# Performance work log

Hardware: AMD Instinct MI355X
Metric: run time of the kernel (lower is better)

The kernel has to match this reference:

```python
import jax, jax.numpy as jnp
import numpy as np

D_MODEL = 2048
NUM_HEADS = 16
D_H = D_MODEL // NUM_HEADS
D_LATENT = 512
B, S = 2, 2048


def setup_inputs() -> dict:
    key = jax.random.key(0)
    ks = jax.random.split(key, 10)
    sd = lambda fan_in: 1.0 / np.sqrt(fan_in)
    x = jax.random.normal(ks[0], (B, S, D_MODEL), dtype=jnp.float32)
    # weights stored as [in, out] so y = x @ W + b (same math as nn.Linear)
    w_latent = jax.random.uniform(ks[1], (D_MODEL, D_LATENT), jnp.float32, -sd(D_MODEL), sd(D_MODEL))
    b_latent = jax.random.uniform(ks[2], (D_LATENT,), jnp.float32, -sd(D_MODEL), sd(D_MODEL))
    w_q = jax.random.uniform(ks[3], (D_MODEL, D_MODEL), jnp.float32, -sd(D_MODEL), sd(D_MODEL))
    b_q = jax.random.uniform(ks[4], (D_MODEL,), jnp.float32, -sd(D_MODEL), sd(D_MODEL))
    # per-head K/V projections batched into [H, d_latent, d_h]
    w_k = jax.random.uniform(ks[5], (NUM_HEADS, D_LATENT, D_H), jnp.float32, -sd(D_LATENT), sd(D_LATENT))
    b_k = jax.random.uniform(ks[6], (NUM_HEADS, D_H), jnp.float32, -sd(D_LATENT), sd(D_LATENT))
    w_v = jax.random.uniform(ks[7], (NUM_HEADS, D_LATENT, D_H), jnp.float32, -sd(D_LATENT), sd(D_LATENT))
    b_v = jax.random.uniform(ks[8], (NUM_HEADS, D_H), jnp.float32, -sd(D_LATENT), sd(D_LATENT))
    w_o = jax.random.uniform(ks[9], (D_MODEL, D_MODEL), jnp.float32, -sd(D_MODEL), sd(D_MODEL))
    b_o = jnp.zeros((D_MODEL,), jnp.float32)
    return {"x": x, "w_latent": w_latent, "b_latent": b_latent, "w_q": w_q, "b_q": b_q,
            "w_k": w_k, "b_k": b_k, "w_v": w_v, "b_v": b_v, "w_o": w_o, "b_o": b_o}


def reference(x, w_latent, b_latent, w_q, b_q, w_k, b_k, w_v, b_v, w_o, b_o):
    batch, seq, d = x.shape
    # latent KV compression: [B,S,d_latent]
    z = x @ w_latent + b_latent
    # queries: [B,H,S,d_h]
    q = (x @ w_q + b_q).reshape(batch, seq, NUM_HEADS, D_H).transpose(0, 2, 1, 3)
    # per-head K/V projections fused into one batched GEMM: [B,H,S,d_h]
    k = jnp.einsum('bsl,hld->bhsd', z, w_k) + b_k[None, :, None, :]
    v = jnp.einsum('bsl,hld->bhsd', z, w_v) + b_v[None, :, None, :]
    attn = jnp.einsum('bhqd,bhkd->bhqk', q, k) / np.sqrt(D_H).astype(np.float32)
    attn = jax.nn.softmax(attn, axis=-1)
    out = jnp.einsum('bhqk,bhkd->bhqd', attn, v)          # [B,H,S,d_h]
    out = out.transpose(0, 2, 1, 3).reshape(batch, seq, d)  # [B,S,D]
    return out @ w_o + b_o
```

## Files before the change

### kernel.cpp

```cpp
#include <hip/hip_runtime.h>
#include <hip/hip_bf16.h>

#define H_ATT   16
#define DH      128
#define DMODEL  2048
#define DLAT    512
#define NB      2
#define SEQ     2048
#define MROWS   (NB * SEQ)
#define NQZ     (DMODEL + DLAT)

#define SCL2 0.12751744f

typedef __bf16          bf16x8_t __attribute__((ext_vector_type(8)));
typedef float           f32x4_t  __attribute__((ext_vector_type(4)));
typedef unsigned short  u16x4_t  __attribute__((ext_vector_type(4)));

#if __has_builtin(__builtin_amdgcn_exp2f)
#define EXP2F(x) __builtin_amdgcn_exp2f(x)
#else
#define EXP2F(x) exp2f(x)
#endif

__device__ __forceinline__ unsigned short f2bf_u16(float f) {
  union { __bf16 b; unsigned short u; } cv; cv.b = (__bf16)f; return cv.u;
}

__device__ __forceinline__ void async_copy16(const __bf16* g, __bf16* l) {
  __builtin_amdgcn_global_load_lds(
      (const __attribute__((address_space(1))) unsigned int*)g,
      (__attribute__((address_space(3))) unsigned int*)l, 16, 0, 0);
}

__global__ void cast_f32_to_bf16(const float* __restrict__ in, __bf16* __restrict__ out, int n4) {
  int i = blockIdx.x * 256 + threadIdx.x;
  if (i >= n4) return;
  float4 v = ((const float4*)in)[i];
  ushort4 o;
  o.x = f2bf_u16(v.x); o.y = f2bf_u16(v.y); o.z = f2bf_u16(v.z); o.w = f2bf_u16(v.w);
  *((ushort4*)out + i) = o;
}

__global__ void transpose_cast(const float* __restrict__ in, __bf16* __restrict__ out,
                               int R, int C, float scale) {
  __shared__ float tile[32][33];
  in  += (size_t)blockIdx.z * R * C;
  out += (size_t)blockIdx.z * R * C;
  int c0 = blockIdx.x * 32, r0 = blockIdx.y * 32;
  int tx = threadIdx.x, ty = threadIdx.y;
  #pragma unroll
  for (int i = 0; i < 32; i += 8)
    tile[ty + i][tx] = in[(size_t)(r0 + ty + i) * C + (c0 + tx)];
  __syncthreads();
  #pragma unroll
  for (int i = 0; i < 32; i += 8)
    out[(size_t)(c0 + ty + i) * R + (r0 + tx)] = (__bf16)(tile[tx][ty + i] * scale);
}

__global__ void build_bqz(const float* __restrict__ b_q, const float* __restrict__ b_lat,
                          float* __restrict__ bqz) {
  int t = blockIdx.x * 256 + threadIdx.x;
  if (t < DMODEL)   bqz[t] = b_q[t] * SCL2;
  else if (t < NQZ) bqz[t] = b_lat[t - DMODEL];
}

#define BM 128
#define BN 128
#define BK 32

__device__ __forceinline__ void storec(float*  p, float v) { *p = v; }
__device__ __forceinline__ void storec(__bf16* p, float v) { *p = (__bf16)v; }

template <typename OutT, bool TRANSPV>
__global__ __launch_bounds__(256, 2)
void gemm_bt(const __bf16* __restrict__ A, const __bf16* __restrict__ Bt,
             const float* __restrict__ bias, OutT* __restrict__ C,
             int M, int N, int K, int lda, int ldc) {
  __shared__ __align__(16) __bf16 As[BM * BK];
  __shared__ __align__(16) __bf16 Bs[BN * BK];
  const int t    = threadIdx.x;
  const int wave = t >> 6, lane = t & 63;
  const int quad = lane >> 4, l16 = lane & 15;
  const int wm = (wave >> 1) * 64, wn = (wave & 1) * 64;
  const int row0 = blockIdx.y * BM, col0 = blockIdx.x * BN;
  const int srow = t >> 2, skc = t & 3;

  const __bf16* Ag  = A  + (size_t)(row0 + srow)      * lda + skc * 8;
  const __bf16* Ag2 = A  + (size_t)(row0 + srow + 64) * lda + skc * 8;
  const __bf16* Bg  = Bt + (size_t)(col0 + srow)      * K   + skc * 8;
  const __bf16* Bg2 = Bt + (size_t)(col0 + srow + 64) * K   + skc * 8;
  __bf16* Al  = As + t * 8;
  __bf16* Al2 = As + 2048 + t * 8;
  __bf16* Bl  = Bs + t * 8;
  __bf16* Bl2 = Bs + 2048 + t * 8;

  f32x4_t acc[4][4] = {};

  for (int k0 = 0; k0 < K; k0 += BK) {
    async_copy16(Ag  + k0, Al);
    async_copy16(Ag2 + k0, Al2);
    async_copy16(Bg  + k0, Bl);
    async_copy16(Bg2 + k0, Bl2);
    __syncthreads();
    bf16x8_t af[4], bfr[4];
    #pragma unroll
    for (int i = 0; i < 4; ++i)
      af[i] = *(const bf16x8_t*)(As + (wm + i * 16 + l16) * BK + quad * 8);
    #pragma unroll
    for (int j = 0; j < 4; ++j)
      bfr[j] = *(const bf16x8_t*)(Bs + (wn + j * 16 + l16) * BK + quad * 8);
    #pragma unroll
    for (int i = 0; i < 4; ++i)
      #pragma unroll
      for (int j = 0; j < 4; ++j)
        acc[i][j] = __builtin_amdgcn_mfma_f32_16x16x32_bf16(af[i], bfr[j], acc[i][j], 0, 0, 0);
    __syncthreads();
  }

  #pragma unroll
  for (int j = 0; j < 4; ++j) {
    int col = col0 + wn + j * 16 + l16;
    float bj = bias[col];
    #pragma unroll
    for (int i = 0; i < 4; ++i) {
      int row = row0 + wm + i * 16 + quad * 4;
      if (TRANSPV) {
        u16x4_t pw;
        #pragma unroll
        for (int r = 0; r < 4; ++r) pw[r] = f2bf_u16(acc[i][j][r] + bj);
        size_t bb = (size_t)(row >> 11);
        int s = row & (SEQ - 1);
        *(u16x4_t*)((__bf16*)C + bb * ((size_t)DMODEL * SEQ) + (size_t)col * SEQ + s) = pw;
      } else {
        #pragma unroll
        for (int r = 0; r < 4; ++r)
          storec(&C[(size_t)(row + r) * ldc + col], acc[i][j][r] + bj);
      }
    }
  }
}

#define TQ 128
#define TK 64

__global__ __launch_bounds__(256, 2)
void mla_attn(const __bf16* __restrict__ Qm, const __bf16* __restrict__ Km,
              const __bf16* __restrict__ Vtg, __bf16* __restrict__ Om) {
  __shared__ __align__(16) __bf16 Kls[16 * 512];
  __shared__ __align__(16) __bf16 Vls[2][16 * 512];
  __shared__ __align__(16) __bf16 Ps [16 * 512];
  __shared__ float Lbuf[2][TQ];

  const int t    = threadIdx.x;
  const int wave = t >> 6, lane = t & 63;
  const int quad = lane >> 4, l16 = lane & 15;
  const int wq = wave >> 1, wk = wave & 1, wd = wave & 1;
  const int h = blockIdx.y, b = blockIdx.z;
  const int q0 = blockIdx.x * TQ;
  const size_t kbase  = (size_t)b * SEQ * DMODEL + (size_t)h * DH;
  const size_t vtbase = ((size_t)b * DMODEL + (size_t)h * DH) * SEQ;
  const size_t obase  = (size_t)b * SEQ * DMODEL + (size_t)h * DH;

  bf16x8_t qf[4][4];
  #pragma unroll
  for (int nt = 0; nt < 4; ++nt) {
    const __bf16* qp = Qm + ((size_t)b * SEQ + q0 + wq * 64 + nt * 16 + l16) * NQZ
                       + (size_t)h * DH + quad * 8;
    #pragma unroll
    for (int kc = 0; kc < 4; ++kc)
      qf[nt][kc] = *(const bf16x8_t*)(qp + kc * 32);
  }

  auto stage = [&](int kt0, int vbuf) {
    #pragma unroll
    for (int i2 = 0; i2 < 4; ++i2) {
      int bidx = wave * 4 + i2;
      int mt = bidx >> 2, kc = bidx & 3;
      async_copy16(Km + kbase + (size_t)(kt0 + mt * 16 + l16) * DMODEL + kc * 32 + quad * 8,
                   Kls + bidx * 512 + lane * 8);
      int dt = bidx >> 1, ks = bidx & 1;
      async_copy16(Vtg + vtbase + (size_t)(dt * 16 + l16) * SEQ + kt0 + ks * 32 + quad * 8,
                   Vls[vbuf] + bidx * 512 + lane * 8);
    }
  };

  f32x4_t acc_o[4][4] = {};
  float l_part[4] = {0.f, 0.f, 0.f, 0.f};

  stage(0, 0);

  f32x4_t acc_s[2][4];
  for (int it = 0; it < SEQ / TK; ++it) {
    __syncthreads();

    if (it > 0) {
      const __bf16* Vb = Vls[(it - 1) & 1];
      #pragma unroll
      for (int ks = 0; ks < 2; ++ks) {
        bf16x8_t pf[4];
        #pragma unroll
        for (int mq = 0; mq < 4; ++mq)
          pf[mq] = *(const bf16x8_t*)(Ps + ((wq * 4 + mq) * 2 + ks) * 512 + lane * 8);
        #pragma unroll
        for (int nd = 0; nd < 4; ++nd) {
          bf16x8_t vf = *(const bf16x8_t*)(Vb + ((wd * 4 + nd) * 2 + ks) * 512 + lane * 8);
          #pragma unroll
          for (int mq = 0; mq < 4; ++mq)
            acc_o[mq][nd] = __builtin_amdgcn_mfma_f32_16x16x32_bf16(pf[mq], vf, acc_o[mq][nd], 0, 0, 0);
        }
      }
    }

    #pragma unroll
    for (int mtl = 0; mtl < 2; ++mtl)
      #pragma unroll
      for (int nt = 0; nt < 4; ++nt)
        acc_s[mtl][nt] = f32x4_t{0.f, 0.f, 0.f, 0.f};
    #pragma unroll
    for (int kc = 0; kc < 4; ++kc)
      #pragma unroll
      for (int mtl = 0; mtl < 2; ++mtl) {
        bf16x8_t kf = *(const bf16x8_t*)(Kls + ((wk * 2 + mtl) * 4 + kc) * 512 + lane * 8);
        #pragma unroll
        for (int nt = 0; nt < 4; ++nt)
          acc_s[mtl][nt] = __builtin_amdgcn_mfma_f32_16x16x32_bf16(kf, qf[nt][kc], acc_s[mtl][nt], 0, 0, 0);
      }

    __syncthreads();

    if (it + 1 < SEQ / TK) stage((it + 1) * TK, (it + 1) & 1);

    #pragma unroll
    for (int nt = 0; nt < 4; ++nt) {
      #pragma unroll
      for (int mtl = 0; mtl < 2; ++mtl) {
        u16x4_t pw;
        float s = 0.f;
        #pragma unroll
        for (int r = 0; r < 4; ++r) {
          float p = EXP2F(fminf(acc_s[mtl][nt][r], 80.f));
          s += p;
          pw[r] = f2bf_u16(p);
        }
        l_part[nt] += s;
        *(u16x4_t*)(Ps + ((wq * 4 + nt) * 2 + wk) * 512
                    + ((mtl * 2 + (quad >> 1)) * 16 + l16) * 8 + (quad & 1) * 4) = pw;
      }
    }
  }

  __syncthreads();
  {
    const __bf16* Vb = Vls[(SEQ / TK - 1) & 1];
    #pragma unroll
    for (int ks = 0; ks < 2; ++ks) {
      bf16x8_t pf[4];
      #pragma unroll
      for (int mq = 0; mq < 4; ++mq)
        pf[mq] = *(const bf16x8_t*)(Ps + ((wq * 4 + mq) * 2 + ks) * 512 + lane * 8);
      #pragma unroll
      for (int nd = 0; nd < 4; ++nd) {
        bf16x8_t vf = *(const bf16x8_t*)(Vb + ((wd * 4 + nd) * 2 + ks) * 512 + lane * 8);
        #pragma unroll
        for (int mq = 0; mq < 4; ++mq)
          acc_o[mq][nd] = __builtin_amdgcn_mfma_f32_16x16x32_bf16(pf[mq], vf, acc_o[mq][nd], 0, 0, 0);
      }
    }
  }

  #pragma unroll
  for (int nt = 0; nt < 4; ++nt) {
    float lp = l_part[nt];
    lp += __shfl_xor(lp, 16);
    lp += __shfl_xor(lp, 32);
    Lbuf[wk][wq * 64 + nt * 16 + l16] = lp;
  }
  __syncthreads();
  #pragma unroll
  for (int mq = 0; mq < 4; ++mq) {
    float li[4];
    #pragma unroll
    for (int r = 0; r < 4; ++r) {
      int qq = wq * 64 + mq * 16 + quad * 4 + r;
      li[r] = 1.f / (Lbuf[0][qq] + Lbuf[1][qq]);
    }
    #pragma unroll
    for (int nd = 0; nd < 4; ++nd) {
      int col = wd * 64 + nd * 16 + l16;
      #pragma unroll
      for (int r = 0; r < 4; ++r) {
        int row = q0 + wq * 64 + mq * 16 + quad * 4 + r;
        Om[obase + (size_t)row * DMODEL + col] = (__bf16)(acc_o[mq][nd][r] * li[r]);
      }
    }
  }
}

extern "C" void kernel_launch(void* const* d_in, const int* in_sizes, int n_in,
                              void* d_out, int out_size, void* d_ws, size_t ws_size,
                              hipStream_t stream) {
  (void)in_sizes; (void)n_in; (void)out_size; (void)ws_size;
  const float* x        = (const float*)d_in[0];
  const float* w_latent = (const float*)d_in[1];
  const float* b_latent = (const float*)d_in[2];
  const float* w_q      = (const float*)d_in[3];
  const float* b_q      = (const float*)d_in[4];
  const float* w_k      = (const float*)d_in[5];
  const float* b_k      = (const float*)d_in[6];
  const float* w_v      = (const float*)d_in[7];
  const float* b_v      = (const float*)d_in[8];
  const float* w_o      = (const float*)d_in[9];
  const float* b_o      = (const float*)d_in[10];
  float* out = (float*)d_out;

  __bf16* ws = (__bf16*)d_ws;
  __bf16* xb   = ws; ws += (size_t)MROWS * DMODEL;
  __bf16* wqzt = ws; ws += (size_t)NQZ * DMODEL;
  __bf16* wkt  = ws; ws += (size_t)DMODEL * DLAT;
  __bf16* wvt  = ws; ws += (size_t)DMODEL * DLAT;
  __bf16* wot  = ws; ws += (size_t)DMODEL * DMODEL;
  __bf16* qzb  = ws; ws += (size_t)MROWS * NQZ;
  __bf16* kb   = ws; ws += (size_t)MROWS * DMODEL;
  __bf16* vt   = ws; ws += (size_t)MROWS * DMODEL;
  __bf16* ao   = ws; ws += (size_t)MROWS * DMODEL;
  float*  bqz  = (float*)ws;

  dim3 blk256(256), blkT(32, 8);
  cast_f32_to_bf16<<<MROWS * DMODEL / 4 / 256, blk256, 0, stream>>>(x, xb, MROWS * DMODEL / 4);
  transpose_cast<<<dim3(DMODEL/32, DMODEL/32, 1),   blkT, 0, stream>>>(w_q,      wqzt,                         DMODEL, DMODEL, SCL2);
  transpose_cast<<<dim3(DLAT/32,   DMODEL/32, 1),   blkT, 0, stream>>>(w_latent, wqzt + (size_t)DMODEL*DMODEL, DMODEL, DLAT,   1.f);
  transpose_cast<<<dim3(DH/32,     DLAT/32, H_ATT), blkT, 0, stream>>>(w_k,      wkt,                          DLAT,   DH,     1.f);
  transpose_cast<<<dim3(DH/32,     DLAT/32, H_ATT), blkT, 0, stream>>>(w_v,      wvt,                          DLAT,   DH,     1.f);
  transpose_cast<<<dim3(DMODEL/32, DMODEL/32, 1),   blkT, 0, stream>>>(w_o,      wot,                          DMODEL, DMODEL, 1.f);
  build_bqz<<<(NQZ + 255) / 256, blk256, 0, stream>>>(b_q, b_latent, bqz);

  gemm_bt<__bf16, false><<<dim3(NQZ/BN, MROWS/BM), blk256, 0, stream>>>(
      xb, wqzt, bqz, qzb, MROWS, NQZ, DMODEL, DMODEL, NQZ);
  gemm_bt<__bf16, false><<<dim3(DMODEL/BN, MROWS/BM), blk256, 0, stream>>>(
      qzb + DMODEL, wkt, b_k, kb, MROWS, DMODEL, DLAT, NQZ, DMODEL);
  gemm_bt<__bf16, true><<<dim3(DMODEL/BN, MROWS/BM), blk256, 0, stream>>>(
      qzb + DMODEL, wvt, b_v, vt, MROWS, DMODEL, DLAT, NQZ, DMODEL);

  mla_attn<<<dim3(SEQ/TQ, H_ATT, NB), blk256, 0, stream>>>(qzb, kb, vt, ao);

  gemm_bt<float, false><<<dim3(DMODEL/BN, MROWS/BM), blk256, 0, stream>>>(
      ao, wot, b_o, out, MROWS, DMODEL, DMODEL, DMODEL, DMODEL);
}
```

Measured before the change: 362.5 us.

## Fuse prep kernels, merge K/V GEMMs, and re-pipeline attention with smaller key tiles

Collapses the cast, weight-transpose and bias-building launches into one multi-role prep kernel. The separate K and V projection GEMMs become one GEMM over a concatenated weight, whose epilogue writes V in transposed layout for the upper column half. The attention kernel drops its key tile from 64 to 32 and uses double-buffered K/P plus triple-buffered V, issuing the next tile's async loads before the current compute so one barrier per iteration suffices. This aims to cut launch overhead and barrier stalls, in exchange for twice as many loop iterations and smaller MFMA batches per step.

New measurement: 386.1 us. 6.5% more time.

```diff
diff --git a/kernel.cpp b/kernel.cpp
--- a/kernel.cpp
+++ b/kernel.cpp
@@ -9,6 +9,7 @@
 #define SEQ     2048
 #define MROWS   (NB * SEQ)
 #define NQZ     (DMODEL + DLAT)
+#define NKV     (2 * DMODEL)
 
 #define SCL2 0.12751744f
 
@@ -32,36 +33,78 @@
       (__attribute__((address_space(3))) unsigned int*)l, 16, 0, 0);
 }
 
-__global__ void cast_f32_to_bf16(const float* __restrict__ in, __bf16* __restrict__ out, int n4) {
-  int i = blockIdx.x * 256 + threadIdx.x;
-  if (i >= n4) return;
-  float4 v = ((const float4*)in)[i];
-  ushort4 o;
-  o.x = f2bf_u16(v.x); o.y = f2bf_u16(v.y); o.z = f2bf_u16(v.z); o.w = f2bf_u16(v.w);
-  *((ushort4*)out + i) = o;
-}
-
-__global__ void transpose_cast(const float* __restrict__ in, __bf16* __restrict__ out,
-                               int R, int C, float scale) {
+#define NB_CAST 8192
+#define NB_WQ   4096
+#define NB_WL   1024
+#define NB_WK   1024
+#define NB_WV   1024
+#define NB_WO   4096
+#define NB_BIAS 26
+#define NB_PREP (NB_CAST + NB_WQ + NB_WL + NB_WK + NB_WV + NB_WO + NB_BIAS)
+
+__global__ void prep(const float* __restrict__ x,
+                     const float* __restrict__ w_q, const float* __restrict__ w_latent,
+                     const float* __restrict__ w_k, const float* __restrict__ w_v,
+                     const float* __restrict__ w_o,
+                     const float* __restrict__ b_q, const float* __restrict__ b_lat,
+                     const float* __restrict__ b_k, const float* __restrict__ b_v,
+                     __bf16* __restrict__ xb, __bf16* __restrict__ wqzt,
+                     __bf16* __restrict__ wkvt, __bf16* __restrict__ wot,
+                     float* __restrict__ bqz, float* __restrict__ bkv) {
   __shared__ float tile[32][33];
-  in  += (size_t)blockIdx.z * R * C;
-  out += (size_t)blockIdx.z * R * C;
-  int c0 = blockIdx.x * 32, r0 = blockIdx.y * 32;
-  int tx = threadIdx.x, ty = threadIdx.y;
-  #pragma unroll
-  for (int i = 0; i < 32; i += 8)
-    tile[ty + i][tx] = in[(size_t)(r0 + ty + i) * C + (c0 + tx)];
+  int bi = blockIdx.x;
+  int t  = threadIdx.x;
+
+  if (bi < NB_CAST) {
+    int i = bi * 256 + t;
+    float4 v = ((const float4*)x)[i];
+    ushort4 o;
+    o.x = f2bf_u16(v.x); o.y = f2bf_u16(v.y); o.z = f2bf_u16(v.z); o.w = f2bf_u16(v.w);
+    ((ushort4*)xb)[i] = o;
+    return;
+  }
+  bi -= NB_CAST;
+
+  const float* in = nullptr; __bf16* out = nullptr;
+  int R = 0, C = 0, bx = 0, by = 0; float scale = 1.f;
+  if (bi < NB_WQ) {
+    in = w_q; out = wqzt; R = DMODEL; C = DMODEL; scale = SCL2;
+    bx = bi & 63; by = bi >> 6;
+  } else if ((bi -= NB_WQ) < NB_WL) {
+    in = w_latent; out = wqzt + (size_t)DMODEL * DMODEL; R = DMODEL; C = DLAT;
+    bx = bi & 15; by = bi >> 4;
+  } else if ((bi -= NB_WL) < NB_WK) {
+    int h = bi >> 6, rem = bi & 63;
+    in = w_k + (size_t)h * DLAT * DH; out = wkvt + (size_t)h * DH * DLAT;
+    R = DLAT; C = DH; bx = rem & 3; by = rem >> 2;
+  } else if ((bi -= NB_WK) < NB_WV) {
+    int h = bi >> 6, rem = bi & 63;
+    in = w_v + (size_t)h * DLAT * DH;
+    out = wkvt + (size_t)DMODEL * DLAT + (size_t)h * DH * DLAT;
+    R = DLAT; C = DH; bx = rem & 3; by = rem >> 2;
+  } else if ((bi -= NB_WV) < NB_WO) {
+    in = w_o; out = wot; R = DMODEL; C = DMODEL;
+    bx = bi & 63; by = bi >> 6;
+  } else {
+    bi -= NB_WO;
+    int idx = bi * 256 + t;
+    if (idx < DMODEL)                bqz[idx] = b_q[idx] * SCL2;
+    else if (idx < NQZ)              bqz[idx] = b_lat[idx - DMODEL];
+    else if (idx < NQZ + DMODEL)     bkv[idx - NQZ] = b_k[idx - NQZ];
+    else if (idx < NQZ + NKV)        bkv[idx - NQZ] = b_v[idx - NQZ - DMODEL];
+    return;
+  }
+
+  int tx = t & 31, ty = t >> 5;
+  const float* ip = in + (size_t)(by * 32) * C + bx * 32;
+  #pragma unroll
+  for (int i = 0; i < 4; ++i)
+    tile[ty + i * 8][tx] = ip[(size_t)(ty + i * 8) * C + tx];
   __syncthreads();
-  #pragma unroll
-  for (int i = 0; i < 32; i += 8)
-    out[(size_t)(c0 + ty + i) * R + (r0 + tx)] = (__bf16)(tile[tx][ty + i] * scale);
-}
-
-__global__ void build_bqz(const float* __restrict__ b_q, const float* __restrict__ b_lat,
-                          float* __restrict__ bqz) {
-  int t = blockIdx.x * 256 + threadIdx.x;
-  if (t < DMODEL)   bqz[t] = b_q[t] * SCL2;
-  else if (t < NQZ) bqz[t] = b_lat[t - DMODEL];
+  __bf16* op = out + (size_t)(bx * 32) * R + by * 32;
+  #pragma unroll
+  for (int i = 0; i < 4; ++i)
+    op[(size_t)(ty + i * 8) * R + tx] = (__bf16)(tile[tx][ty + i * 8] * scale);
 }
 
 #define BM 128
@@ -71,10 +114,11 @@
 __device__ __forceinline__ void storec(float*  p, float v) { *p = v; }
 __device__ __forceinline__ void storec(__bf16* p, float v) { *p = (__bf16)v; }
 
-template <typename OutT, bool TRANSPV>
+template <typename OutT, bool KVDUAL>
 __global__ __launch_bounds__(256, 2)
 void gemm_bt(const __bf16* __restrict__ A, const __bf16* __restrict__ Bt,
              const float* __restrict__ bias, OutT* __restrict__ C,
+             __bf16* __restrict__ Cvt,
              int M, int N, int K, int lda, int ldc) {
   __shared__ __align__(16) __bf16 As[BM * BK];
   __shared__ __align__(16) __bf16 Bs[BN * BK];
@@ -117,6 +161,7 @@
     __syncthreads();
   }
 
+  const bool vmode = KVDUAL && (col0 >= DMODEL);
   #pragma unroll
   for (int j = 0; j < 4; ++j) {
     int col = col0 + wn + j * 16 + l16;
@@ -124,13 +169,13 @@
     #pragma unroll
     for (int i = 0; i < 4; ++i) {
       int row = row0 + wm + i * 16 + quad * 4;
-      if (TRANSPV) {
+      if (vmode) {
         u16x4_t pw;
         #pragma unroll
         for (int r = 0; r < 4; ++r) pw[r] = f2bf_u16(acc[i][j][r] + bj);
         size_t bb = (size_t)(row >> 11);
         int s = row & (SEQ - 1);
-        *(u16x4_t*)((__bf16*)C + bb * ((size_t)DMODEL * SEQ) + (size_t)col * SEQ + s) = pw;
+        *(u16x4_t*)(Cvt + bb * ((size_t)DMODEL * SEQ) + (size_t)(col - DMODEL) * SEQ + s) = pw;
       } else {
         #pragma unroll
         for (int r = 0; r < 4; ++r)
@@ -141,14 +186,14 @@
 }
 
 #define TQ 128
-#define TK 64
+#define TK 32
 
 __global__ __launch_bounds__(256, 2)
 void mla_attn(const __bf16* __restrict__ Qm, const __bf16* __restrict__ Km,
               const __bf16* __restrict__ Vtg, __bf16* __restrict__ Om) {
-  __shared__ __align__(16) __bf16 Kls[16 * 512];
-  __shared__ __align__(16) __bf16 Vls[2][16 * 512];
-  __shared__ __align__(16) __bf16 Ps [16 * 512];
+  __shared__ __align__(16) __bf16 Kls[2][8 * 512];
+  __shared__ __align__(16) __bf16 Vls[3][8 * 512];
+  __shared__ __align__(16) __bf16 Ps [2][8 * 512];
   __shared__ float Lbuf[2][TQ];
 
   const int t    = threadIdx.x;
@@ -171,102 +216,74 @@
       qf[nt][kc] = *(const bf16x8_t*)(qp + kc * 32);
   }
 
-  auto stage = [&](int kt0, int vbuf) {
-    #pragma unroll
-    for (int i2 = 0; i2 < 4; ++i2) {
-      int bidx = wave * 4 + i2;
+  auto stage = [&](int tile) {
+    int kt0 = tile * TK;
+    __bf16* Kd = Kls[tile & 1];
+    __bf16* Vd = Vls[tile % 3];
+    #pragma unroll
+    for (int i2 = 0; i2 < 2; ++i2) {
+      int bidx = wave * 2 + i2;
       int mt = bidx >> 2, kc = bidx & 3;
       async_copy16(Km + kbase + (size_t)(kt0 + mt * 16 + l16) * DMODEL + kc * 32 + quad * 8,
-                   Kls + bidx * 512 + lane * 8);
-      int dt = bidx >> 1, ks = bidx & 1;
-      async_copy16(Vtg + vtbase + (size_t)(dt * 16 + l16) * SEQ + kt0 + ks * 32 + quad * 8,
-                   Vls[vbuf] + bidx * 512 + lane * 8);
+                   Kd + bidx * 512 + lane * 8);
+      async_copy16(Vtg + vtbase + (size_t)(bidx * 16 + l16) * SEQ + kt0 + quad * 8,
+                   Vd + bidx * 512 + lane * 8);
     }
   };
 
   f32x4_t acc_o[4][4] = {};
   float l_part[4] = {0.f, 0.f, 0.f, 0.f};
 
-  stage(0, 0);
-
-  f32x4_t acc_s[2][4];
+  auto pv = [&](const __bf16* Pd, const __bf16* Vd) {
+    bf16x8_t pf[4];
+    #pragma unroll
+    for (int mq = 0; mq < 4; ++mq)
+      pf[mq] = *(const bf16x8_t*)(Pd + (wq * 4 + mq) * 512 + lane * 8);
+    #pragma unroll
+    for (int nd = 0; nd < 4; ++nd) {
+      bf16x8_t vf = *(const bf16x8_t*)(Vd + (wd * 4 + nd) * 512 + lane * 8);
+      #pragma unroll
+      for (int mq = 0; mq < 4; ++mq)
+        acc_o[mq][nd] = __builtin_amdgcn_mfma_f32_16x16x32_bf16(pf[mq], vf, acc_o[mq][nd], 0, 0, 0);
+    }
+  };
+
+  stage(0);
+
   for (int it = 0; it < SEQ / TK; ++it) {
     __syncthreads();
-
-    if (it > 0) {
-      const __bf16* Vb = Vls[(it - 1) & 1];
-      #pragma unroll
-      for (int ks = 0; ks < 2; ++ks) {
-        bf16x8_t pf[4];
-        #pragma unroll
-        for (int mq = 0; mq < 4; ++mq)
-          pf[mq] = *(const bf16x8_t*)(Ps + ((wq * 4 + mq) * 2 + ks) * 512 + lane * 8);
-        #pragma unroll
-        for (int nd = 0; nd < 4; ++nd) {
-          bf16x8_t vf = *(const bf16x8_t*)(Vb + ((wd * 4 + nd) * 2 + ks) * 512 + lane * 8);
-          #pragma unroll
-          for (int mq = 0; mq < 4; ++mq)
-            acc_o[mq][nd] = __builtin_amdgcn_mfma_f32_16x16x32_bf16(pf[mq], vf, acc_o[mq][nd], 0, 0, 0);
-        }
+    if (it + 1 < SEQ / TK) stage(it + 1);
+    if (it > 0) pv(Ps[(it - 1) & 1], Vls[(it - 1) % 3]);
+
+    f32x4_t acc_s[4] = {};
+    const __bf16* Kb = Kls[it & 1];
+    #pragma unroll
+    for (int kc = 0; kc < 4; ++kc) {
+      bf16x8_t kf = *(const bf16x8_t*)(Kb + (wk * 4 + kc) * 512 + lane * 8);
+      #pragma unroll
+      for (int nt = 0; nt < 4; ++nt)
+        acc_s[nt] = __builtin_amdgcn_mfma_f32_16x16x32_bf16(kf, qf[nt][kc], acc_s[nt], 0, 0, 0);
+    }
+
+    __bf16* Pd = Ps[it & 1];
+    #pragma unroll
+    for (int nt = 0; nt < 4; ++nt) {
+      u16x4_t pw;
+      float s = 0.f;
+      #pragma unroll
+      for (int r = 0; r < 4; ++r) {
+        float p = EXP2F(fminf(acc_s[nt][r], 80.f));
+        s += p;
+        pw[r] = f2bf_u16(p);
       }
-    }
-
-    #pragma unroll
-    for (int mtl = 0; mtl < 2; ++mtl)
-      #pragma unroll
-      for (int nt = 0; nt < 4; ++nt)
-        acc_s[mtl][nt] = f32x4_t{0.f, 0.f, 0.f, 0.f};
-    #pragma unroll
-    for (int kc = 0; kc < 4; ++kc)
-      #pragma unroll
-      for (int mtl = 0; mtl < 2; ++mtl) {
-        bf16x8_t kf = *(const bf16x8_t*)(Kls + ((wk * 2 + mtl) * 4 + kc) * 512 + lane * 8);
-        #pragma unroll
-        for (int nt = 0; nt < 4; ++nt)
-          acc_s[mtl][nt] = __builtin_amdgcn_mfma_f32_16x16x32_bf16(kf, qf[nt][kc], acc_s[mtl][nt], 0, 0, 0);
-      }
-
-    __syncthreads();
-
-    if (it + 1 < SEQ / TK) stage((it + 1) * TK, (it + 1) & 1);
-
-    #pragma unroll
-    for (int nt = 0; nt < 4; ++nt) {
-      #pragma unroll
-      for (int mtl = 0; mtl < 2; ++mtl) {
-        u16x4_t pw;
-        float s = 0.f;
-        #pragma unroll
-        for (int r = 0; r < 4; ++r) {
-          float p = EXP2F(fminf(acc_s[mtl][nt][r], 80.f));
-          s += p;
-          pw[r] = f2bf_u16(p);
-        }
-        l_part[nt] += s;
-        *(u16x4_t*)(Ps + ((wq * 4 + nt) * 2 + wk) * 512
-                    + ((mtl * 2 + (quad >> 1)) * 16 + l16) * 8 + (quad & 1) * 4) = pw;
-      }
+      l_part[nt] += s;
+      *(u16x4_t*)(Pd + (wq * 4 + nt) * 512
+                  + ((wk * 2 + (quad >> 1)) * 16 + l16) * 8 + (quad & 1) * 4) = pw;
     }
   }
 
   __syncthreads();
-  {
-    const __bf16* Vb = Vls[(SEQ / TK - 1) & 1];
-    #pragma unroll
-    for (int ks = 0; ks < 2; ++ks) {
-      bf16x8_t pf[4];
-      #pragma unroll
-      for (int mq = 0; mq < 4; ++mq)
-        pf[mq] = *(const bf16x8_t*)(Ps + ((wq * 4 + mq) * 2 + ks) * 512 + lane * 8);
-      #pragma unroll
-      for (int nd = 0; nd < 4; ++nd) {
-        bf16x8_t vf = *(const bf16x8_t*)(Vb + ((wd * 4 + nd) * 2 + ks) * 512 + lane * 8);
-        #pragma unroll
-        for (int mq = 0; mq < 4; ++mq)
-          acc_o[mq][nd] = __builtin_amdgcn_mfma_f32_16x16x32_bf16(pf[mq], vf, acc_o[mq][nd], 0, 0, 0);
-      }
-    }
-  }
+  pv(Ps[(SEQ / TK - 1) & 1], Vls[(SEQ / TK - 1) % 3]);
 
   #pragma unroll
   for (int nt = 0; nt < 4; ++nt) {
@@ -316,33 +333,27 @@
   __bf16* ws = (__bf16*)d_ws;
   __bf16* xb   = ws; ws += (size_t)MROWS * DMODEL;
   __bf16* wqzt = ws; ws += (size_t)NQZ * DMODEL;
-  __bf16* wkt  = ws; ws += (size_t)DMODEL * DLAT;
-  __bf16* wvt  = ws; ws += (size_t)DMODEL * DLAT;
+  __bf16* wkvt = ws; ws += (size_t)NKV * DLAT;
   __bf16* wot  = ws; ws += (size_t)DMODEL * DMODEL;
   __bf16* qzb  = ws; ws += (size_t)MROWS * NQZ;
   __bf16* kb   = ws; ws += (size_t)MROWS * DMODEL;
   __bf16* vt   = ws; ws += (size_t)MROWS * DMODEL;
   __bf16* ao   = ws; ws += (size_t)MROWS * DMODEL;
   float*  bqz  = (float*)ws;
-
-  dim3 blk256(256), blkT(32, 8);
-  cast_f32_to_bf16<<<MROWS * DMODEL / 4 / 256, blk256, 0, stream>>>(x, xb, MROWS * DMODEL / 4);
-  transpose_cast<<<dim3(DMODEL/32, DMODEL/32, 1),   blkT, 0, stream>>>(w_q,      wqzt,                         DMODEL, DMODEL, SCL2);
-  transpose_cast<<<dim3(DLAT/32,   DMODEL/32, 1),   blkT, 0, stream>>>(w_latent, wqzt + (size_t)DMODEL*DMODEL, DMODEL, DLAT,   1.f);
-  transpose_cast<<<dim3(DH/32,     DLAT/32, H_ATT), blkT, 0, stream>>>(w_k,      wkt,                          DLAT,   DH,     1.f);
-  transpose_cast<<<dim3(DH/32,     DLAT/32, H_ATT), blkT, 0, stream>>>(w_v,      wvt,                          DLAT,   DH,     1.f);
-  transpose_cast<<<dim3(DMODEL/32, DMODEL/32, 1),   blkT, 0, stream>>>(w_o,      wot,                          DMODEL, DMODEL, 1.f);
-  build_bqz<<<(NQZ + 255) / 256, blk256, 0, stream>>>(b_q, b_latent, bqz);
+  float*  bkv  = bqz + NQZ;
+
+  dim3 blk256(256);
+  prep<<<NB_PREP, blk256, 0, stream>>>(x, w_q, w_latent, w_k, w_v, w_o,
+                                       b_q, b_latent, b_k, b_v,
+                                       xb, wqzt, wkvt, wot, bqz, bkv);
 
   gemm_bt<__bf16, false><<<dim3(NQZ/BN, MROWS/BM), blk256, 0, stream>>>(
-      xb, wqzt, bqz, qzb, MROWS, NQZ, DMODEL, DMODEL, NQZ);
-  gemm_bt<__bf16, false><<<dim3(DMODEL/BN, MROWS/BM), blk256, 0, stream>>>(
-      qzb + DMODEL, wkt, b_k, kb, MROWS, DMODEL, DLAT, NQZ, DMODEL);
-  gemm_bt<__bf16, true><<<dim3(DMODEL/BN, MROWS/BM), blk256, 0, stream>>>(
-      qzb + DMODEL, wvt, b_v, vt, MROWS, DMODEL, DLAT, NQZ, DMODEL);
+      xb, wqzt, bqz, qzb, nullptr, MROWS, NQZ, DMODEL, DMODEL, NQZ);
+  gemm_bt<__bf16, true><<<dim3(NKV/BN, MROWS/BM), blk256, 0, stream>>>(
+      qzb + DMODEL, wkvt, bkv, kb, vt, MROWS, NKV, DLAT, NQZ, DMODEL);
 
   mla_attn<<<dim3(SEQ/TQ, H_ATT, NB), blk256, 0, stream>>>(qzb, kb, vt, ao);
 
   gemm_bt<float, false><<<dim3(DMODEL/BN, MROWS/BM), blk256, 0, stream>>>(
-      ao, wot, b_o, out, MROWS, DMODEL, DMODEL, DMODEL, DMODEL);
-}
+      ao, wot, b_o, out, nullptr, MROWS, DMODEL, DMODEL, DMODEL, DMODEL);
+}
```
